# Kernel tuning notes

Measured on AMD Instinct MI355X. Metric: run time of the kernel, lower is better.

## Reference

```python
import jax, jax.numpy as jnp
import numpy as np

# Static graph structure: gene nodes first, GO-term nodes last (mask is sorted).
N_GENE, N_GOID = 40000, 10000
N = N_GENE + N_GOID
E = 800000
INPUT_DIM, H1, H2, OUT_DIM, GOID_DIM = 1280, 256, 128, 64, 4096


def setup_inputs() -> dict:
    key = jax.random.key(0)
    ks = jax.random.split(key, 16)
    s = 0.02
    return {
        "x": jax.random.normal(ks[0], (N, GOID_DIM), jnp.float32),
        "edge_index": jax.random.randint(ks[1], (2, E), 0, N),
        "mask": jnp.concatenate([jnp.ones(N_GENE, bool), jnp.zeros(N_GOID, bool)]),
        # goid_dnn: Linear(4096,1024) -> ReLU -> Linear(1024,INPUT_DIM) -> ReLU
        "Wd1": jax.random.normal(ks[2], (GOID_DIM, 1024), jnp.float32) * s,
        "bd1": jnp.zeros((1024,), jnp.float32),
        "Wd2": jax.random.normal(ks[3], (1024, INPUT_DIM), jnp.float32) * s,
        "bd2": jnp.zeros((INPUT_DIM,), jnp.float32),
        # GCNConv layers
        "W1": jax.random.normal(ks[4], (INPUT_DIM, H1), jnp.float32) * s,
        "b1": jnp.zeros((H1,), jnp.float32),
        "W2": jax.random.normal(ks[5], (H1, H2), jnp.float32) * s,
        "b2": jnp.zeros((H2,), jnp.float32),
        # goid projections
        "Wp1": jax.random.normal(ks[6], (INPUT_DIM, H1), jnp.float32) * s,
        "bp1": jnp.zeros((H1,), jnp.float32),
        "Wp2": jax.random.normal(ks[7], (H1, H2), jnp.float32) * s,
        "bp2": jnp.zeros((H2,), jnp.float32),
        # final fc
        "Wf": jax.random.normal(ks[8], (H2, OUT_DIM), jnp.float32) * s,
        "bf": jnp.zeros((OUT_DIM,), jnp.float32),
    }


def gcn_conv(x, W, b, src, dst):
    """PyG GCNConv: xW, then sym-normalized (A + I) aggregation, then bias."""
    # degree over targets with self-loops already appended to (src, dst)
    deg = jax.ops.segment_sum(jnp.ones_like(dst, x.dtype), dst, num_segments=N)
    dinv = jnp.where(deg > 0, jax.lax.rsqrt(deg), 0.0)
    norm = dinv[src] * dinv[dst]                       # [E+N]
    xw = x @ W                                          # [N, F_out]
    msg = xw[src] * norm[:, None]                       # gather-scale, [E+N, F_out]
    return jax.ops.segment_sum(msg, dst, num_segments=N) + b


def reference(x, edge_index, mask, Wd1, bd1, Wd2, bd2, W1, b1, W2, b2,
              Wp1, bp1, Wp2, bp2, Wf, bf):
    del mask  # structurally: first N_GENE rows are genes, rest are GO terms
    loop = jnp.arange(N, dtype=edge_index.dtype)
    src = jnp.concatenate([edge_index[0], loop])
    dst = jnp.concatenate([edge_index[1], loop])

    gene_x = x[:N_GENE, :INPUT_DIM]
    goid_x = x[N_GENE:]
    # goid_dnn runs under torch.no_grad() -> stop_gradient
    goid_t = jax.lax.stop_gradient(
        jax.nn.relu(jax.nn.relu(goid_x @ Wd1 + bd1) @ Wd2 + bd2))

    x_t = jnp.concatenate([gene_x, goid_t], axis=0)      # [N, INPUT_DIM]
    h1 = jax.nn.relu(gcn_conv(x_t, W1, b1, src, dst))    # dropout disabled (eval)
    p1 = goid_t @ Wp1 + bp1                              # goid_proj1
    h1 = h1.at[N_GENE:].set(p1)                          # masked scatter assign
    h2 = jax.nn.relu(gcn_conv(h1, W2, b2, src, dst))
    h2 = h2.at[N_GENE:].set(p1 @ Wp2 + bp2)              # goid_proj2(goid_proj1(...))
    return h2 @ Wf + bf                                  # [N, OUT_DIM]
```

## Files before the change

### kernel.cpp

```cpp
#include <hip/hip_runtime.h>

constexpr int kNGene = 40000;
constexpr int kNGoid = 10000;
constexpr int kN     = 50000;
constexpr int kE     = 800000;
constexpr int kInDim = 1280;
constexpr int kH1    = 256;
constexpr int kH2    = 128;
constexpr int kOut   = 64;
constexpr int kGDim  = 4096;
constexpr int kD1    = 1024;

typedef short bf16x8 __attribute__((ext_vector_type(8)));
typedef float f32x4  __attribute__((ext_vector_type(4)));

static __device__ __forceinline__ short f2bf(float f) {
  union { float f; unsigned u; } v; v.f = f;
  unsigned r = v.u + 0x7FFF + ((v.u >> 16) & 1);
  return (short)(r >> 16);
}
static __device__ __forceinline__ float bf2f(short s) {
  union { unsigned u; float f; } v;
  v.u = ((unsigned)(unsigned short)s) << 16;
  return v.f;
}
static __device__ __forceinline__ void gld16(const void* g, void* l) {
  __builtin_amdgcn_global_load_lds(
      (const __attribute__((address_space(1))) void*)g,
      (__attribute__((address_space(3))) void*)l, 16, 0, 0);
}
template <int N>
static __device__ __forceinline__ void wait_barrier() {
  if constexpr (N == 0)      asm volatile("s_waitcnt vmcnt(0)" ::: "memory");
  else if constexpr (N == 3) asm volatile("s_waitcnt vmcnt(3)" ::: "memory");
  else                       asm volatile("s_waitcnt vmcnt(4)" ::: "memory");
  __builtin_amdgcn_s_barrier();
  asm volatile("" ::: "memory");
}

constexpr int kCvtBlocks   = 20000;
constexpr int kTransBlocks = 6088;
constexpr int kInitBlocks  = 196;

__global__ __launch_bounds__(256)
void k_prep(const float* __restrict__ goid_x, short* __restrict__ goidx_bf,
            const float* __restrict__ Wd1, short* __restrict__ Wd1t,
            const float* __restrict__ Wd2, short* __restrict__ Wd2t,
            const float* __restrict__ W1,  short* __restrict__ W1t,
            const float* __restrict__ Wp1, short* __restrict__ Wp1t,
            const float* __restrict__ W2,  short* __restrict__ W2t,
            const float* __restrict__ Wp2, short* __restrict__ Wp2t,
            const float* __restrict__ Wf,  short* __restrict__ Wft,
            float* __restrict__ deg, int* __restrict__ gcount)
{
  __shared__ float t[32][33];
  int b = blockIdx.x;
  if (b < kCvtBlocks) {
    int idx = b * 256 + threadIdx.x;
    int r = idx >> 9;
    int c = (idx & 511) << 3;
    const float* sp = goid_x + (size_t)r * kGDim + c;
    float4 v0 = *reinterpret_cast<const float4*>(sp);
    float4 v1 = *reinterpret_cast<const float4*>(sp + 4);
    bf16x8 o;
    o[0]=f2bf(v0.x); o[1]=f2bf(v0.y); o[2]=f2bf(v0.z); o[3]=f2bf(v0.w);
    o[4]=f2bf(v1.x); o[5]=f2bf(v1.y); o[6]=f2bf(v1.z); o[7]=f2bf(v1.w);
    *reinterpret_cast<bf16x8*>(goidx_bf + (size_t)r * kGDim + c) = o;
    return;
  }
  if (b >= kCvtBlocks + kTransBlocks) {
    int i = (b - kCvtBlocks - kTransBlocks) * 256 + threadIdx.x;
    if (i < kN) deg[i] = 1.0f;
    if (i == 0) *gcount = 0;
    return;
  }
  int b2 = b - kCvtBlocks;
  const float* W; short* Wt; int K, N, bi;
  if (b2 < 4096)      { W = Wd1; Wt = Wd1t; K = 4096; N = 1024; bi = b2; }
  else if (b2 < 5376) { W = Wd2; Wt = Wd2t; K = 1024; N = 1280; bi = b2 - 4096; }
  else if (b2 < 5696) { W = W1;  Wt = W1t;  K = 1280; N = 256;  bi = b2 - 5376; }
  else if (b2 < 6016) { W = Wp1; Wt = Wp1t; K = 1280; N = 256;  bi = b2 - 5696; }
  else if (b2 < 6048) { W = W2;  Wt = W2t;  K = 256;  N = 128;  bi = b2 - 6016; }
  else if (b2 < 6080) { W = Wp2; Wt = Wp2t; K = 256;  N = 128;  bi = b2 - 6048; }
  else                { W = Wf;  Wt = Wft;  K = 128;  N = 64;   bi = b2 - 6080; }
  int nbx = N >> 5;
  int n0 = (bi % nbx) * 32, k0 = (bi / nbx) * 32;
  int tx = threadIdx.x & 31, ty = threadIdx.x >> 5;
#pragma unroll
  for (int p = 0; p < 4; ++p)
    t[ty + 8 * p][tx] = W[(size_t)(k0 + ty + 8 * p) * N + n0 + tx];
  __syncthreads();
#pragma unroll
  for (int p = 0; p < 4; ++p)
    Wt[(size_t)(n0 + ty + 8 * p) * K + k0 + tx] = f2bf(t[tx][ty + 8 * p]);
}

__global__ void k_deg_hist(const int* __restrict__ ei, float* __restrict__ deg) {
  int e = blockIdx.x * blockDim.x + threadIdx.x;
  if (e < kE) atomicAdd(&deg[ei[kE + e]], 1.0f);
}
__global__ void k_rowassign(const float* __restrict__ deg, int* __restrict__ rowstart,
                            int* __restrict__ cursor, int* __restrict__ gcount) {
  int i = blockIdx.x * blockDim.x + threadIdx.x;
  int lane = threadIdx.x & 63;
  int c = (i < kNGene) ? ((int)deg[i] - 1) : 0;
  int incl = c;
#pragma unroll
  for (int off = 1; off < 64; off <<= 1) {
    int t = __shfl_up(incl, off, 64);
    if (lane >= off) incl += t;
  }
  int total = __shfl(incl, 63, 64);
  int base = 0;
  if (lane == 63) base = atomicAdd(gcount, total);
  base = __shfl(base, 63, 64);
  if (i < kNGene) {
    int s = base + incl - c;
    rowstart[i] = s;
    cursor[i] = s;
  }
}
__global__ void k_fill(const int* __restrict__ ei, const float* __restrict__ deg,
                       int* __restrict__ cursor, int2* __restrict__ edges) {
  int e = blockIdx.x * blockDim.x + threadIdx.x;
  if (e >= kE) return;
  int dst = ei[kE + e];
  if (dst >= kNGene) return;
  int src = ei[e];
  int pos = atomicAdd(&cursor[dst], 1);
  float nrm = rsqrtf(deg[src] * deg[dst]);
  edges[pos] = make_int2(src, __float_as_int(nrm));
}

template <int F, int OBF>
__global__ __launch_bounds__(256)
void k_gather_bf(const short* __restrict__ xw, const float* __restrict__ deg,
                 const int* __restrict__ rowstart, const int2* __restrict__ edges,
                 const float* __restrict__ bias, void* __restrict__ hv) {
  constexpr int VEC = F / 64;
  int row = (blockIdx.x * blockDim.x + threadIdx.x) >> 6;
  int lane = threadIdx.x & 63;
  if (row >= kNGene) return;
  float dg = deg[row];
  float inv = 1.0f / dg;
  float acc[VEC];
  {
    const short* xr = xw + (size_t)row * F + lane * VEC;
    if constexpr (VEC == 4) {
      short4 s = *reinterpret_cast<const short4*>(xr);
      acc[0] = bf2f(s.x) * inv; acc[1] = bf2f(s.y) * inv;
      acc[2] = bf2f(s.z) * inv; acc[3] = bf2f(s.w) * inv;
    } else {
      short2 s = *reinterpret_cast<const short2*>(xr);
      acc[0] = bf2f(s.x) * inv; acc[1] = bf2f(s.y) * inv;
    }
  }
  const int2* ep = edges + rowstart[row];
  int n = (int)dg - 1;
  int e = 0;
  for (; e + 1 < n; e += 2) {
    int2 p0 = ep[e], p1 = ep[e + 1];
    float n0 = __int_as_float(p0.y), n1 = __int_as_float(p1.y);
    const short* x0 = xw + (size_t)p0.x * F + lane * VEC;
    const short* x1 = xw + (size_t)p1.x * F + lane * VEC;
    if constexpr (VEC == 4) {
      short4 s0 = *reinterpret_cast<const short4*>(x0);
      short4 s1 = *reinterpret_cast<const short4*>(x1);
      acc[0] += bf2f(s0.x) * n0; acc[1] += bf2f(s0.y) * n0;
      acc[2] += bf2f(s0.z) * n0; acc[3] += bf2f(s0.w) * n0;
      acc[0] += bf2f(s1.x) * n1; acc[1] += bf2f(s1.y) * n1;
      acc[2] += bf2f(s1.z) * n1; acc[3] += bf2f(s1.w) * n1;
    } else {
      short2 s0 = *reinterpret_cast<const short2*>(x0);
      short2 s1 = *reinterpret_cast<const short2*>(x1);
      acc[0] += bf2f(s0.x) * n0; acc[1] += bf2f(s0.y) * n0;
      acc[0] += bf2f(s1.x) * n1; acc[1] += bf2f(s1.y) * n1;
    }
  }
  if (e < n) {
    int2 p0 = ep[e];
    float n0 = __int_as_float(p0.y);
    const short* x0 = xw + (size_t)p0.x * F + lane * VEC;
    if constexpr (VEC == 4) {
      short4 s0 = *reinterpret_cast<const short4*>(x0);
      acc[0] += bf2f(s0.x) * n0; acc[1] += bf2f(s0.y) * n0;
      acc[2] += bf2f(s0.z) * n0; acc[3] += bf2f(s0.w) * n0;
    } else {
      short2 s0 = *reinterpret_cast<const short2*>(x0);
      acc[0] += bf2f(s0.x) * n0; acc[1] += bf2f(s0.y) * n0;
    }
  }
#pragma unroll
  for (int v = 0; v < VEC; ++v) acc[v] = fmaxf(acc[v] + bias[lane * VEC + v], 0.f);
  if constexpr (OBF) {
    short* hp = (short*)hv + (size_t)row * F + lane * VEC;
    if constexpr (VEC == 4) {
      short4 o; o.x = f2bf(acc[0]); o.y = f2bf(acc[1]); o.z = f2bf(acc[2]); o.w = f2bf(acc[3]);
      *reinterpret_cast<short4*>(hp) = o;
    } else {
      short2 o; o.x = f2bf(acc[0]); o.y = f2bf(acc[1]);
      *reinterpret_cast<short2*>(hp) = o;
    }
  } else {
    float* hp = (float*)hv + (size_t)row * F + lane * VEC;
    if constexpr (VEC == 4) {
      float4 o; o.x = acc[0]; o.y = acc[1]; o.z = acc[2]; o.w = acc[3];
      *reinterpret_cast<float4*>(hp) = o;
    } else {
      float2 o; o.x = acc[0]; o.y = acc[1];
      *reinterpret_cast<float2*>(hp) = o;
    }
  }
}

template <int RELU, int OBF>
__global__ __launch_bounds__(256)
void k_gemm_bf16a(const short* __restrict__ A, int lda,
                  const short* __restrict__ Bt,
                  const float* __restrict__ bias,
                  void* __restrict__ Cv, int ldc,
                  int M, int K)
{
  __shared__ __align__(16) short As[3][128 * 32];
  __shared__ __align__(16) short Bs[3][128 * 32];
  const int tid  = threadIdx.x;
  const int lane = tid & 63;
  const int wid  = tid >> 6;
  const int wr = wid >> 1, wc = wid & 1;
  const int row0 = blockIdx.y * 128;
  const int col0 = blockIdx.x * 128;
  const int l15 = lane & 15, l4 = lane >> 4;
  const int srow = lane >> 2;
  const int schunk = (lane & 3) ^ ((lane >> 3) & 3);
  const int rslot8 = (l4 ^ ((l15 >> 1) & 3)) * 8;

  f32x4 acc[4][4] = {};

  auto stage = [&](int buf, int k0) {
#pragma unroll
    for (int q = 0; q < 2; ++q) {
      int seg = wid * 2 + q;
      int r = seg * 16 + srow;
      int grow = row0 + r;
      if (grow >= M) grow = M - 1;
      gld16(A + (size_t)grow * lda + k0 + schunk * 8, &As[buf][seg * 512]);
      int gcol = col0 + r;
      gld16(Bt + (size_t)gcol * K + k0 + schunk * 8, &Bs[buf][seg * 512]);
    }
  };

  const int nt = K >> 5;
  stage(0, 0);
  if (nt > 1) { stage(1, 32); wait_barrier<4>(); }
  else        { wait_barrier<0>(); }

  for (int t = 0; t < nt; ++t) {
    if (t + 2 < nt) stage((t + 2) % 3, (t + 2) * 32);
    const int cur = t % 3;
    bf16x8 af[4], bfr[4];
#pragma unroll
    for (int m = 0; m < 4; ++m)
      af[m] = *reinterpret_cast<bf16x8*>(&As[cur][(wr * 64 + m * 16 + l15) * 32 + rslot8]);
#pragma unroll
    for (int n = 0; n < 4; ++n)
      bfr[n] = *reinterpret_cast<bf16x8*>(&Bs[cur][(wc * 64 + n * 16 + l15) * 32 + rslot8]);
#pragma unroll
    for (int m = 0; m < 4; ++m)
#pragma unroll
      for (int n = 0; n < 4; ++n)
        acc[m][n] = __builtin_amdgcn_mfma_f32_16x16x32_bf16(af[m], bfr[n], acc[m][n], 0, 0, 0);
    if (t + 1 < nt) {
      if (t + 2 < nt) wait_barrier<4>(); else wait_barrier<0>();
    }
  }

#pragma unroll
  for (int n = 0; n < 4; ++n) {
    int col = col0 + wc * 64 + n * 16 + l15;
    float bv = bias ? bias[col] : 0.f;
#pragma unroll
    for (int m = 0; m < 4; ++m) {
      int rb = row0 + wr * 64 + m * 16 + l4 * 4;
#pragma unroll
      for (int e = 0; e < 4; ++e) {
        int r = rb + e;
        if (r < M) {
          float v = acc[m][n][e] + bv;
          if (RELU) v = fmaxf(v, 0.f);
          size_t idx = (size_t)r * ldc + col;
          if constexpr (OBF) ((short*)Cv)[idx] = f2bf(v);
          else               ((float*)Cv)[idx] = v;
        }
      }
    }
  }
}

template <int RELU, int OBF>
__global__ __launch_bounds__(512)
void k_gemm_wide(const short* __restrict__ A, int lda,
                 const short* __restrict__ Bt,
                 const float* __restrict__ bias,
                 void* __restrict__ Cv, int ldc,
                 int M, int K)
{
  __shared__ __align__(16) short As[3][128 * 32];
  __shared__ __align__(16) short Bs[3][256 * 32];
  const int tid  = threadIdx.x;
  const int lane = tid & 63;
  const int wid  = tid >> 6;
  const int wr = wid >> 2, wc = wid & 3;
  int nwg = gridDim.x * gridDim.y;
  int b0 = blockIdx.y * gridDim.x + blockIdx.x;
  int qq = nwg >> 3, rr = nwg & 7, xcd = b0 & 7, j = b0 >> 3;
  int swz = ((xcd < rr) ? xcd * (qq + 1) : rr * (qq + 1) + (xcd - rr) * qq) + j;
  const int row0 = (swz / gridDim.x) * 128;
  const int col0 = (swz % gridDim.x) * 256;
  const int l15 = lane & 15, l4 = lane >> 4;
  const int srow = lane >> 2;
  const int schunk = (lane & 3) ^ ((lane >> 3) & 3);
  const int rslot8 = (l4 ^ ((l15 >> 1) & 3)) * 8;

  f32x4 acc[4][4] = {};

  auto stage = [&](int buf, int k0) {
#pragma unroll
    for (int q = 0; q < 3; ++q) {
      int s = wid * 3 + q;
      if (s < 8) {
        int grow = row0 + s * 16 + srow;
        if (grow >= M) grow = M - 1;
        gld16(A + (size_t)grow * lda + k0 + schunk * 8, &As[buf][s * 512]);
      } else {
        int gcol = col0 + (s - 8) * 16 + srow;
        gld16(Bt + (size_t)gcol * K + k0 + schunk * 8, &Bs[buf][(s - 8) * 512]);
      }
    }
  };

  const int nt = K >> 5;
  stage(0, 0);
  if (nt > 1) { stage(1, 32); wait_barrier<3>(); }
  else        { wait_barrier<0>(); }

  for (int t = 0; t < nt; ++t) {
    if (t + 2 < nt) stage((t + 2) % 3, (t + 2) * 32);
    const int cur = t % 3;
    bf16x8 af[4], bfr[4];
#pragma unroll
    for (int m = 0; m < 4; ++m)
      af[m] = *reinterpret_cast<bf16x8*>(&As[cur][(wr * 64 + m * 16 + l15) * 32 + rslot8]);
#pragma unroll
    for (int n = 0; n < 4; ++n)
      bfr[n] = *reinterpret_cast<bf16x8*>(&Bs[cur][(wc * 64 + n * 16 + l15) * 32 + rslot8]);
#pragma unroll
    for (int m = 0; m < 4; ++m)
#pragma unroll
      for (int n = 0; n < 4; ++n)
        acc[m][n] = __builtin_amdgcn_mfma_f32_16x16x32_bf16(af[m], bfr[n], acc[m][n], 0, 0, 0);
    if (t + 1 < nt) {
      if (t + 2 < nt) wait_barrier<3>(); else wait_barrier<0>();
    }
  }

#pragma unroll
  for (int n = 0; n < 4; ++n) {
    int col = col0 + wc * 64 + n * 16 + l15;
    float bv = bias ? bias[col] : 0.f;
#pragma unroll
    for (int m = 0; m < 4; ++m) {
      int rb = row0 + wr * 64 + m * 16 + l4 * 4;
#pragma unroll
      for (int e = 0; e < 4; ++e) {
        int r = rb + e;
        if (r < M) {
          float v = acc[m][n][e] + bv;
          if (RELU) v = fmaxf(v, 0.f);
          size_t idx = (size_t)r * ldc + col;
          if constexpr (OBF) ((short*)Cv)[idx] = f2bf(v);
          else               ((float*)Cv)[idx] = v;
        }
      }
    }
  }
}

__global__ __launch_bounds__(512)
void k_combo_wide(const short* __restrict__ A, int lda,
                  const short* __restrict__ Bt,
                  const float* __restrict__ bp1,
                  short* __restrict__ X1, short* __restrict__ H1,
                  int M, int K)
{
  __shared__ __align__(16) short As[2][128 * 32];
  __shared__ __align__(16) short Bs[2][256 * 32];
  const int tid  = threadIdx.x;
  const int lane = tid & 63;
  const int wid  = tid >> 6;
  const int wr = wid >> 2, wc = wid & 3;
  const int row0 = blockIdx.y * 128;
  const int col0 = blockIdx.x * 256;
  const int l15 = lane & 15, l4 = lane >> 4;
  const int srow = lane >> 2;
  const int schunk = (lane & 3) ^ ((lane >> 3) & 3);
  const int rslot8 = (l4 ^ ((l15 >> 1) & 3)) * 8;

  f32x4 acc[4][4] = {};

  auto stage = [&](int buf, int k0) {
#pragma unroll
    for (int q = 0; q < 3; ++q) {
      int s = wid * 3 + q;
      if (s < 8) {
        int grow = row0 + s * 16 + srow;
        if (grow >= M) grow = M - 1;
        gld16(A + (size_t)grow * lda + k0 + schunk * 8, &As[buf][s * 512]);
      } else {
        int gcol = col0 + (s - 8) * 16 + srow;
        gld16(Bt + (size_t)gcol * K + k0 + schunk * 8, &Bs[buf][(s - 8) * 512]);
      }
    }
  };

  stage(0, 0);
  __syncthreads();
  int cur = 0;
  for (int k0 = 0; k0 < K; k0 += 32) {
    if (k0 + 32 < K) stage(cur ^ 1, k0 + 32);
    bf16x8 af[4], bfr[4];
#pragma unroll
    for (int m = 0; m < 4; ++m)
      af[m] = *reinterpret_cast<bf16x8*>(&As[cur][(wr * 64 + m * 16 + l15) * 32 + rslot8]);
#pragma unroll
    for (int n = 0; n < 4; ++n)
      bfr[n] = *reinterpret_cast<bf16x8*>(&Bs[cur][(wc * 64 + n * 16 + l15) * 32 + rslot8]);
#pragma unroll
    for (int m = 0; m < 4; ++m)
#pragma unroll
      for (int n = 0; n < 4; ++n)
        acc[m][n] = __builtin_amdgcn_mfma_f32_16x16x32_bf16(af[m], bfr[n], acc[m][n], 0, 0, 0);
    __syncthreads();
    cur ^= 1;
  }

  const int is_p1 = (col0 >= 256);
  short* dstp = is_p1 ? H1 : X1;
#pragma unroll
  for (int n = 0; n < 4; ++n) {
    int cl = wc * 64 + n * 16 + l15;
    float bv = is_p1 ? bp1[cl] : 0.f;
#pragma unroll
    for (int m = 0; m < 4; ++m) {
      int rb = row0 + wr * 64 + m * 16 + l4 * 4;
#pragma unroll
      for (int e = 0; e < 4; ++e) {
        int r = rb + e;
        if (r < M) dstp[(size_t)r * 256 + cl] = f2bf(acc[m][n][e] + bv);
      }
    }
  }
}

__global__ __launch_bounds__(512)
void k_gemm_gene(const float* __restrict__ A, int lda,
                 const short* __restrict__ Bt,
                 short* __restrict__ C,
                 int M, int K)
{
  __shared__ short As[2][128 * 40];
  __shared__ __align__(16) short Bs[2][256 * 32];
  const int tid  = threadIdx.x;
  const int lane = tid & 63;
  const int wid  = tid >> 6;
  const int wr = wid >> 2, wc = wid & 3;
  const int row0 = blockIdx.x * 128;
  const int l15 = lane & 15, l4 = lane >> 4;
  const int sr = tid >> 2, sc = tid & 3;
  const int srow = lane >> 2;
  const int schunk = (lane & 3) ^ ((lane >> 3) & 3);
  const int rslot8 = (l4 ^ ((l15 >> 1) & 3)) * 8;

  f32x4 acc[4][4] = {};

  auto stageB = [&](int buf, int k0) {
#pragma unroll
    for (int q = 0; q < 2; ++q) {
      int seg = wid * 2 + q;
      int gcol = seg * 16 + srow;
      gld16(Bt + (size_t)gcol * K + k0 + schunk * 8, &Bs[buf][seg * 512]);
    }
  };
  auto stageA = [&](int buf, int k0) {
    int grow = row0 + sr;
    float4 v0 = make_float4(0.f,0.f,0.f,0.f), v1 = v0;
    if (grow < M) {
      const float* ap = A + (size_t)grow * lda + k0 + sc * 8;
      v0 = *reinterpret_cast<const float4*>(ap);
      v1 = *reinterpret_cast<const float4*>(ap + 4);
    }
    bf16x8 t;
    t[0]=f2bf(v0.x); t[1]=f2bf(v0.y); t[2]=f2bf(v0.z); t[3]=f2bf(v0.w);
    t[4]=f2bf(v1.x); t[5]=f2bf(v1.y); t[6]=f2bf(v1.z); t[7]=f2bf(v1.w);
    *reinterpret_cast<bf16x8*>(&As[buf][sr * 40 + sc * 8]) = t;
  };

  stageB(0, 0); stageA(0, 0);
  __syncthreads();
  int cur = 0;
  for (int k0 = 0; k0 < K; k0 += 32) {
    if (k0 + 32 < K) { stageB(cur ^ 1, k0 + 32); stageA(cur ^ 1, k0 + 32); }
    bf16x8 af[4], bfr[4];
#pragma unroll
    for (int m = 0; m < 4; ++m)
      af[m] = *reinterpret_cast<bf16x8*>(&As[cur][(wr * 64 + m * 16 + l15) * 40 + l4 * 8]);
#pragma unroll
    for (int n = 0; n < 4; ++n)
      bfr[n] = *reinterpret_cast<bf16x8*>(&Bs[cur][(wc * 64 + n * 16 + l15) * 32 + rslot8]);
#pragma unroll
    for (int m = 0; m < 4; ++m)
#pragma unroll
      for (int n = 0; n < 4; ++n)
        acc[m][n] = __builtin_amdgcn_mfma_f32_16x16x32_bf16(af[m], bfr[n], acc[m][n], 0, 0, 0);
    __syncthreads();
    cur ^= 1;
  }

#pragma unroll
  for (int n = 0; n < 4; ++n) {
    int col = wc * 64 + n * 16 + l15;
#pragma unroll
    for (int m = 0; m < 4; ++m) {
      int rb = row0 + wr * 64 + m * 16 + l4 * 4;
#pragma unroll
      for (int e = 0; e < 4; ++e) {
        int r = rb + e;
        if (r < M) C[(size_t)r * 256 + col] = f2bf(acc[m][n][e]);
      }
    }
  }
}

__global__ __launch_bounds__(256)
void k_gemm_out(const short* __restrict__ A,
                const short* __restrict__ Bt,
                const float* __restrict__ bias,
                float* __restrict__ C,
                int M)
{
  __shared__ __align__(16) short As[2][256 * 32];
  __shared__ __align__(16) short Bs[2][64 * 32];
  const int tid  = threadIdx.x;
  const int lane = tid & 63;
  const int wid  = tid >> 6;
  const int row0 = blockIdx.x * 256;
  const int l15 = lane & 15, l4 = lane >> 4;
  const int srow = lane >> 2;
  const int schunk = (lane & 3) ^ ((lane >> 3) & 3);
  const int rslot8 = (l4 ^ ((l15 >> 1) & 3)) * 8;

  f32x4 acc[4][4] = {};

  auto stage = [&](int buf, int k0) {
#pragma unroll
    for (int q = 0; q < 4; ++q) {
      int seg = wid * 4 + q;
      int grow = row0 + seg * 16 + srow;
      if (grow >= M) grow = M - 1;
      gld16(A + (size_t)grow * 128 + k0 + schunk * 8, &As[buf][seg * 512]);
    }
    int gcol = wid * 16 + srow;
    gld16(Bt + (size_t)gcol * 128 + k0 + schunk * 8, &Bs[buf][wid * 512]);
  };

  stage(0, 0);
  __syncthreads();
  int cur = 0;
  for (int k0 = 0; k0 < 128; k0 += 32) {
    if (k0 + 32 < 128) stage(cur ^ 1, k0 + 32);
    bf16x8 af[4], bfr[4];
#pragma unroll
    for (int m = 0; m < 4; ++m)
      af[m] = *reinterpret_cast<bf16x8*>(&As[cur][(wid * 64 + m * 16 + l15) * 32 + rslot8]);
#pragma unroll
    for (int n = 0; n < 4; ++n)
      bfr[n] = *reinterpret_cast<bf16x8*>(&Bs[cur][(n * 16 + l15) * 32 + rslot8]);
#pragma unroll
    for (int m = 0; m < 4; ++m)
#pragma unroll
      for (int n = 0; n < 4; ++n)
        acc[m][n] = __builtin_amdgcn_mfma_f32_16x16x32_bf16(af[m], bfr[n], acc[m][n], 0, 0, 0);
    __syncthreads();
    cur ^= 1;
  }

#pragma unroll
  for (int n = 0; n < 4; ++n) {
    int col = n * 16 + l15;
    float bv = bias[col];
#pragma unroll
    for (int m = 0; m < 4; ++m) {
      int rb = row0 + wid * 64 + m * 16 + l4 * 4;
#pragma unroll
      for (int e = 0; e < 4; ++e) {
        int r = rb + e;
        if (r < M) C[(size_t)r * 64 + col] = acc[m][n][e] + bv;
      }
    }
  }
}

extern "C" void kernel_launch(void* const* d_in, const int* in_sizes, int n_in,
                              void* d_out, int out_size, void* d_ws, size_t ws_size,
                              hipStream_t stream) {
  const float* x   = (const float*)d_in[0];
  const int*   ei  = (const int*)d_in[1];
  const float* Wd1 = (const float*)d_in[3];
  const float* bd1 = (const float*)d_in[4];
  const float* Wd2 = (const float*)d_in[5];
  const float* bd2 = (const float*)d_in[6];
  const float* W1  = (const float*)d_in[7];
  const float* b1  = (const float*)d_in[8];
  const float* W2  = (const float*)d_in[9];
  const float* b2  = (const float*)d_in[10];
  const float* Wp1 = (const float*)d_in[11];
  const float* bp1 = (const float*)d_in[12];
  const float* Wp2 = (const float*)d_in[13];
  const float* bp2 = (const float*)d_in[14];
  const float* Wf  = (const float*)d_in[15];
  const float* bf_ = (const float*)d_in[16];
  float* out = (float*)d_out;
  float* ws  = (float*)d_ws;

  short* goidx_bf = (short*)(ws + 0);
  short* goidt_bf = (short*)(ws + 20480000);
  short* h1tmp_bf = (short*)(ws + 26880000);
  short* Wd1t = (short*)(ws + 32000000);
  short* Wd2t = (short*)(ws + 34097152);
  short* W1t  = (short*)(ws + 34752512);
  short* Wp1t = (short*)(ws + 34916352);
  short* W2t  = (short*)(ws + 35080192);
  short* xw1_bf = (short*)(ws + 35100000);
  short* h1bf   = (short*)(ws + 41500000);
  short* xw2_bf = (short*)(ws + 50460000);
  short* h2bf   = (short*)(ws + 53660000);
  float* deg    = ws + 60060000;
  int*   rowstart = (int*)(ws + 60150016);
  int*   cursor   = (int*)(ws + 60190016);
  int2*  edges    = (int2*)(ws + 60230016);
  int*   gcount   = (int*)(ws + 61830016);
  short* Wp2t = (short*)(ws + 61830032);
  short* Wft  = (short*)(ws + 61846416);

  const float* gene_x = x;
  const float* goid_x = x + (size_t)kNGene * kGDim;

  auto gb = [](int M, int Ncol) { return dim3((unsigned)(Ncol / 128), (unsigned)((M + 127) / 128)); };
  auto gw = [](int M, int Ncol) { return dim3((unsigned)(Ncol / 256), (unsigned)((M + 127) / 128)); };

  k_prep<<<kCvtBlocks + kTransBlocks + kInitBlocks, 256, 0, stream>>>(
      goid_x, goidx_bf, Wd1, Wd1t, Wd2, Wd2t, W1, W1t, Wp1, Wp1t,
      W2, W2t, Wp2, Wp2t, Wf, Wft, deg, gcount);

  k_deg_hist<<<(kE + 255) / 256, 256, 0, stream>>>(ei, deg);
  k_rowassign<<<(kNGene + 255) / 256, 256, 0, stream>>>(deg, rowstart, cursor, gcount);
  k_fill<<<(kE + 255) / 256, 256, 0, stream>>>(ei, deg, cursor, edges);

  k_gemm_wide<1,1><<<gw(kNGoid, kD1), 512, 0, stream>>>(goidx_bf, kGDim, Wd1t, bd1,
                                                        h1tmp_bf, kD1, kNGoid, kGDim);
  k_gemm_wide<1,1><<<gw(kNGoid, kInDim), 512, 0, stream>>>(h1tmp_bf, kD1, Wd2t, bd2,
                                                           goidt_bf, kInDim, kNGoid, kD1);

  k_gemm_gene<<<dim3((kNGene + 127) / 128), 512, 0, stream>>>(gene_x, kGDim, W1t,
                                                              xw1_bf, kNGene, kInDim);

  k_combo_wide<<<dim3(2, (kNGoid + 127) / 128), 512, 0, stream>>>(
      goidt_bf, kInDim, W1t , bp1,
      xw1_bf + (size_t)kNGene * kH1, h1bf + (size_t)kNGene * kH1,
      kNGoid, kInDim);

  k_gather_bf<kH1,1><<<(kNGene * 64 + 255) / 256, 256, 0, stream>>>(
      xw1_bf, deg, rowstart, edges, b1, h1bf);

  k_gemm_bf16a<0,1><<<gb(kN, kH2), 256, 0, stream>>>(h1bf, kH1, W2t, nullptr,
                                                     xw2_bf, kH2, kN, kH1);

  k_gather_bf<kH2,1><<<(kNGene * 64 + 255) / 256, 256, 0, stream>>>(
      xw2_bf, deg, rowstart, edges, b2, h2bf);
  k_gemm_bf16a<0,1><<<gb(kNGoid, kH2), 256, 0, stream>>>(
      h1bf + (size_t)kNGene * kH1, kH1, Wp2t, bp2,
      h2bf + (size_t)kNGene * kH2, kH2, kNGoid, kH1);

  k_gemm_out<<<(kN + 255) / 256, 256, 0, stream>>>(h2bf, Wft, bf_, out, kN);
}
```

Before: 603.3 us.

## Merge independent GEMMs and graph-build kernels into combined heterogeneous launches

Independent stages are packed into single launches with per-block dispatch: the Wd1 GEMM, gene GEMM and degree histogram share one kernel; the Wd2 GEMM shares one with row assignment; the combo GEMM shares one with CSR fill; and the W2 and Wp2 GEMMs are merged. This cuts launch count and lets the light atomic work overlap the GEMMs instead of running serially. In exchange, the Wd GEMMs lose their triple-buffered pipeline and use a double-buffered loop with full barriers. Dynamic shared memory sized for the largest branch may also lower occupancy for the light blocks.

```diff
diff --git a/kernel.cpp b/kernel.cpp
--- a/kernel.cpp
+++ b/kernel.cpp
@@ -95,13 +95,16 @@
     Wt[(size_t)(n0 + ty + 8 * p) * K + k0 + tx] = f2bf(t[tx][ty + 8 * p]);
 }
 
-__global__ void k_deg_hist(const int* __restrict__ ei, float* __restrict__ deg) {
-  int e = blockIdx.x * blockDim.x + threadIdx.x;
+static __device__ void dev_hist(const int* __restrict__ ei, float* __restrict__ deg,
+                                int bid) {
+  int e = bid * 512 + threadIdx.x;
   if (e < kE) atomicAdd(&deg[ei[kE + e]], 1.0f);
 }
-__global__ void k_rowassign(const float* __restrict__ deg, int* __restrict__ rowstart,
-                            int* __restrict__ cursor, int* __restrict__ gcount) {
-  int i = blockIdx.x * blockDim.x + threadIdx.x;
+static __device__ void dev_rowassign(const float* __restrict__ deg,
+                                     int* __restrict__ rowstart,
+                                     int* __restrict__ cursor,
+                                     int* __restrict__ gcount, int bid) {
+  int i = bid * 512 + threadIdx.x;
   int lane = threadIdx.x & 63;
   int c = (i < kNGene) ? ((int)deg[i] - 1) : 0;
   int incl = c;
@@ -120,9 +123,10 @@
     cursor[i] = s;
   }
 }
-__global__ void k_fill(const int* __restrict__ ei, const float* __restrict__ deg,
-                       int* __restrict__ cursor, int2* __restrict__ edges) {
-  int e = blockIdx.x * blockDim.x + threadIdx.x;
+static __device__ void dev_fill(const int* __restrict__ ei, const float* __restrict__ deg,
+                                int* __restrict__ cursor, int2* __restrict__ edges,
+                                int bid) {
+  int e = bid * 512 + threadIdx.x;
   if (e >= kE) return;
   int dst = ei[kE + e];
   if (dst >= kNGene) return;
@@ -214,21 +218,21 @@
 }
 
 template <int RELU, int OBF>
-__global__ __launch_bounds__(256)
-void k_gemm_bf16a(const short* __restrict__ A, int lda,
-                  const short* __restrict__ Bt,
-                  const float* __restrict__ bias,
-                  void* __restrict__ Cv, int ldc,
-                  int M, int K)
-{
-  __shared__ __align__(16) short As[3][128 * 32];
-  __shared__ __align__(16) short Bs[3][128 * 32];
+static __device__ void dev_wide(const short* __restrict__ A, int lda,
+                                const short* __restrict__ Bt,
+                                const float* __restrict__ bias,
+                                void* __restrict__ Cv, int ldc,
+                                int M, int K, int b0, int nbx, int nwg,
+                                short* As, short* Bs)
+{
   const int tid  = threadIdx.x;
   const int lane = tid & 63;
   const int wid  = tid >> 6;
-  const int wr = wid >> 1, wc = wid & 1;
-  const int row0 = blockIdx.y * 128;
-  const int col0 = blockIdx.x * 128;
+  const int wr = wid >> 2, wc = wid & 3;
+  int qq = nwg >> 3, rr = nwg & 7, xcd = b0 & 7, j = b0 >> 3;
+  int swz = ((xcd < rr) ? xcd * (qq + 1) : rr * (qq + 1) + (xcd - rr) * qq) + j;
+  const int row0 = (swz / nbx) * 128;
+  const int col0 = (swz % nbx) * 256;
   const int l15 = lane & 15, l4 = lane >> 4;
   const int srow = lane >> 2;
   const int schunk = (lane & 3) ^ ((lane >> 3) & 3);
@@ -238,40 +242,38 @@
 
   auto stage = [&](int buf, int k0) {
 #pragma unroll
-    for (int q = 0; q < 2; ++q) {
-      int seg = wid * 2 + q;
-      int r = seg * 16 + srow;
-      int grow = row0 + r;
-      if (grow >= M) grow = M - 1;
-      gld16(A + (size_t)grow * lda + k0 + schunk * 8, &As[buf][seg * 512]);
-      int gcol = col0 + r;
-      gld16(Bt + (size_t)gcol * K + k0 + schunk * 8, &Bs[buf][seg * 512]);
+    for (int q = 0; q < 3; ++q) {
+      int s = wid * 3 + q;
+      if (s < 8) {
+        int grow = row0 + s * 16 + srow;
+        if (grow >= M) grow = M - 1;
+        gld16(A + (size_t)grow * lda + k0 + schunk * 8, As + buf * 4096 + s * 512);
+      } else {
+        int gcol = col0 + (s - 8) * 16 + srow;
+        gld16(Bt + (size_t)gcol * K + k0 + schunk * 8, Bs + buf * 8192 + (s - 8) * 512);
+      }
     }
   };
 
-  const int nt = K >> 5;
   stage(0, 0);
-  if (nt > 1) { stage(1, 32); wait_barrier<4>(); }
-  else        { wait_barrier<0>(); }
-
-  for (int t = 0; t < nt; ++t) {
-    if (t + 2 < nt) stage((t + 2) % 3, (t + 2) * 32);
-    const int cur = t % 3;
+  __syncthreads();
+  int cur = 0;
+  for (int k0 = 0; k0 < K; k0 += 32) {
+    if (k0 + 32 < K) stage(cur ^ 1, k0 + 32);
     bf16x8 af[4], bfr[4];
 #pragma unroll
     for (int m = 0; m < 4; ++m)
-      af[m] = *reinterpret_cast<bf16x8*>(&As[cur][(wr * 64 + m * 16 + l15) * 32 + rslot8]);
+      af[m] = *reinterpret_cast<bf16x8*>(As + cur * 4096 + (wr * 64 + m * 16 + l15) * 32 + rslot8);
 #pragma unroll
     for (int n = 0; n < 4; ++n)
-      bfr[n] = *reinterpret_cast<bf16x8*>(&Bs[cur][(wc * 64 + n * 16 + l15) * 32 + rslot8]);
+      bfr[n] = *reinterpret_cast<bf16x8*>(Bs + cur * 8192 + (wc * 64 + n * 16 + l15) * 32 + rslot8);
 #pragma unroll
     for (int m = 0; m < 4; ++m)
 #pragma unroll
       for (int n = 0; n < 4; ++n)
         acc[m][n] = __builtin_amdgcn_mfma_f32_16x16x32_bf16(af[m], bfr[n], acc[m][n], 0, 0, 0);
-    if (t + 1 < nt) {
-      if (t + 2 < nt) wait_barrier<4>(); else wait_barrier<0>();
-    }
+    __syncthreads();
+    cur ^= 1;
   }
 
 #pragma unroll
@@ -296,26 +298,95 @@
   }
 }
 
-template <int RELU, int OBF>
-__global__ __launch_bounds__(512)
-void k_gemm_wide(const short* __restrict__ A, int lda,
-                 const short* __restrict__ Bt,
-                 const float* __restrict__ bias,
-                 void* __restrict__ Cv, int ldc,
-                 int M, int K)
-{
-  __shared__ __align__(16) short As[3][128 * 32];
-  __shared__ __align__(16) short Bs[3][256 * 32];
+static __device__ void dev_gene(const float* __restrict__ A, int lda,
+                                const short* __restrict__ Bt,
+                                short* __restrict__ C, int M, int K,
+                                int bx, short* As, short* Bs)
+{
   const int tid  = threadIdx.x;
   const int lane = tid & 63;
   const int wid  = tid >> 6;
   const int wr = wid >> 2, wc = wid & 3;
-  int nwg = gridDim.x * gridDim.y;
-  int b0 = blockIdx.y * gridDim.x + blockIdx.x;
-  int qq = nwg >> 3, rr = nwg & 7, xcd = b0 & 7, j = b0 >> 3;
-  int swz = ((xcd < rr) ? xcd * (qq + 1) : rr * (qq + 1) + (xcd - rr) * qq) + j;
-  const int row0 = (swz / gridDim.x) * 128;
-  const int col0 = (swz % gridDim.x) * 256;
+  const int row0 = bx * 128;
+  const int l15 = lane & 15, l4 = lane >> 4;
+  const int sr = tid >> 2, sc = tid & 3;
+  const int srow = lane >> 2;
+  const int schunk = (lane & 3) ^ ((lane >> 3) & 3);
+  const int rslot8 = (l4 ^ ((l15 >> 1) & 3)) * 8;
+
+  f32x4 acc[4][4] = {};
+
+  auto stageB = [&](int buf, int k0) {
+#pragma unroll
+    for (int q = 0; q < 2; ++q) {
+      int seg = wid * 2 + q;
+      int gcol = seg * 16 + srow;
+      gld16(Bt + (size_t)gcol * K + k0 + schunk * 8, Bs + buf * 8192 + seg * 512);
+    }
+  };
+  auto stageA = [&](int buf, int k0) {
+    int grow = row0 + sr;
+    float4 v0 = make_float4(0.f,0.f,0.f,0.f), v1 = v0;
+    if (grow < M) {
+      const float* ap = A + (size_t)grow * lda + k0 + sc * 8;
+      v0 = *reinterpret_cast<const float4*>(ap);
+      v1 = *reinterpret_cast<const float4*>(ap + 4);
+    }
+    bf16x8 t;
+    t[0]=f2bf(v0.x); t[1]=f2bf(v0.y); t[2]=f2bf(v0.z); t[3]=f2bf(v0.w);
+    t[4]=f2bf(v1.x); t[5]=f2bf(v1.y); t[6]=f2bf(v1.z); t[7]=f2bf(v1.w);
+    *reinterpret_cast<bf16x8*>(As + buf * 5120 + sr * 40 + sc * 8) = t;
+  };
+
+  stageB(0, 0); stageA(0, 0);
+  __syncthreads();
+  int cur = 0;
+  for (int k0 = 0; k0 < K; k0 += 32) {
+    if (k0 + 32 < K) { stageB(cur ^ 1, k0 + 32); stageA(cur ^ 1, k0 + 32); }
+    bf16x8 af[4], bfr[4];
+#pragma unroll
+    for (int m = 0; m < 4; ++m)
+      af[m] = *reinterpret_cast<bf16x8*>(As + cur * 5120 + (wr * 64 + m * 16 + l15) * 40 + l4 * 8);
+#pragma unroll
+    for (int n = 0; n < 4; ++n)
+      bfr[n] = *reinterpret_cast<bf16x8*>(Bs + cur * 8192 + (wc * 64 + n * 16 + l15) * 32 + rslot8);
+#pragma unroll
+    for (int m = 0; m < 4; ++m)
+#pragma unroll
+      for (int n = 0; n < 4; ++n)
+        acc[m][n] = __builtin_amdgcn_mfma_f32_16x16x32_bf16(af[m], bfr[n], acc[m][n], 0, 0, 0);
+    __syncthreads();
+    cur ^= 1;
+  }
+
+#pragma unroll
+  for (int n = 0; n < 4; ++n) {
+    int col = wc * 64 + n * 16 + l15;
+#pragma unroll
+    for (int m = 0; m < 4; ++m) {
+      int rb = row0 + wr * 64 + m * 16 + l4 * 4;
+#pragma unroll
+      for (int e = 0; e < 4; ++e) {
+        int r = rb + e;
+        if (r < M) C[(size_t)r * 256 + col] = f2bf(acc[m][n][e]);
+      }
+    }
+  }
+}
+
+static __device__ void dev_combo(const short* __restrict__ A, int lda,
+                                 const short* __restrict__ Bt,
+                                 const float* __restrict__ bp1,
+                                 short* __restrict__ X1, short* __restrict__ H1,
+                                 int M, int K, int bx, int by,
+                                 short* As, short* Bs)
+{
+  const int tid  = threadIdx.x;
+  const int lane = tid & 63;
+  const int wid  = tid >> 6;
+  const int wr = wid >> 2, wc = wid & 3;
+  const int row0 = by * 128;
+  const int col0 = bx * 256;
   const int l15 = lane & 15, l4 = lane >> 4;
   const int srow = lane >> 2;
   const int schunk = (lane & 3) ^ ((lane >> 3) & 3);
@@ -330,17 +401,90 @@
       if (s < 8) {
         int grow = row0 + s * 16 + srow;
         if (grow >= M) grow = M - 1;
-        gld16(A + (size_t)grow * lda + k0 + schunk * 8, &As[buf][s * 512]);
+        gld16(A + (size_t)grow * lda + k0 + schunk * 8, As + buf * 4096 + s * 512);
       } else {
         int gcol = col0 + (s - 8) * 16 + srow;
-        gld16(Bt + (size_t)gcol * K + k0 + schunk * 8, &Bs[buf][(s - 8) * 512]);
+        gld16(Bt + (size_t)gcol * K + k0 + schunk * 8, Bs + buf * 8192 + (s - 8) * 512);
       }
+    }
+  };
+
+  stage(0, 0);
+  __syncthreads();
+  int cur = 0;
+  for (int k0 = 0; k0 < K; k0 += 32) {
+    if (k0 + 32 < K) stage(cur ^ 1, k0 + 32);
+    bf16x8 af[4], bfr[4];
+#pragma unroll
+    for (int m = 0; m < 4; ++m)
+      af[m] = *reinterpret_cast<bf16x8*>(As + cur * 4096 + (wr * 64 + m * 16 + l15) * 32 + rslot8);
+#pragma unroll
+    for (int n = 0; n < 4; ++n)
+      bfr[n] = *reinterpret_cast<bf16x8*>(Bs + cur * 8192 + (wc * 64 + n * 16 + l15) * 32 + rslot8);
+#pragma unroll
+    for (int m = 0; m < 4; ++m)
+#pragma unroll
+      for (int n = 0; n < 4; ++n)
+        acc[m][n] = __builtin_amdgcn_mfma_f32_16x16x32_bf16(af[m], bfr[n], acc[m][n], 0, 0, 0);
+    __syncthreads();
+    cur ^= 1;
+  }
+
+  const int is_p1 = (col0 >= 256);
+  short* dstp = is_p1 ? H1 : X1;
+#pragma unroll
+  for (int n = 0; n < 4; ++n) {
+    int cl = wc * 64 + n * 16 + l15;
+    float bv = is_p1 ? bp1[cl] : 0.f;
+#pragma unroll
+    for (int m = 0; m < 4; ++m) {
+      int rb = row0 + wr * 64 + m * 16 + l4 * 4;
+#pragma unroll
+      for (int e = 0; e < 4; ++e) {
+        int r = rb + e;
+        if (r < M) dstp[(size_t)r * 256 + cl] = f2bf(acc[m][n][e] + bv);
+      }
+    }
+  }
+}
+
+template <int RELU, int OBF>
+static __device__ void dev_bf16a(const short* __restrict__ A, int lda,
+                                 const short* __restrict__ Bt,
+                                 const float* __restrict__ bias,
+                                 void* __restrict__ Cv, int ldc,
+                                 int M, int K, int bx, int by,
+                                 short* As, short* Bs)
+{
+  const int tid  = threadIdx.x;
+  const int lane = tid & 63;
+  const int wid  = tid >> 6;
+  const int wr = wid >> 1, wc = wid & 1;
+  const int row0 = by * 128;
+  const int col0 = bx * 128;
+  const int l15 = lane & 15, l4 = lane >> 4;
+  const int srow = lane >> 2;
+  const int schunk = (lane & 3) ^ ((lane >> 3) & 3);
+  const int rslot8 = (l4 ^ ((l15 >> 1) & 3)) * 8;
+
+  f32x4 acc[4][4] = {};
+
+  auto stage = [&](int buf, int k0) {
+#pragma unroll
+    for (int q = 0; q < 2; ++q) {
+      int seg = wid * 2 + q;
+      int r = seg * 16 + srow;
+      int grow = row0 + r;
+      if (grow >= M) grow = M - 1;
+      gld16(A + (size_t)grow * lda + k0 + schunk * 8, As + buf * 4096 + seg * 512);
+      int gcol = col0 + r;
+      gld16(Bt + (size_t)gcol * K + k0 + schunk * 8, Bs + buf * 4096 + seg * 512);
     }
   };
 
   const int nt = K >> 5;
   stage(0, 0);
-  if (nt > 1) { stage(1, 32); wait_barrier<3>(); }
+  if (nt > 1) { stage(1, 32); wait_barrier<4>(); }
   else        { wait_barrier<0>(); }
 
   for (int t = 0; t < nt; ++t) {
@@ -349,17 +493,17 @@
     bf16x8 af[4], bfr[4];
 #pragma unroll
     for (int m = 0; m < 4; ++m)
-      af[m] = *reinterpret_cast<bf16x8*>(&As[cur][(wr * 64 + m * 16 + l15) * 32 + rslot8]);
+      af[m] = *reinterpret_cast<bf16x8*>(As + cur * 4096 + (wr * 64 + m * 16 + l15) * 32 + rslot8);
 #pragma unroll
     for (int n = 0; n < 4; ++n)
-      bfr[n] = *reinterpret_cast<bf16x8*>(&Bs[cur][(wc * 64 + n * 16 + l15) * 32 + rslot8]);
+      bfr[n] = *reinterpret_cast<bf16x8*>(Bs + cur * 4096 + (wc * 64 + n * 16 + l15) * 32 + rslot8);
 #pragma unroll
     for (int m = 0; m < 4; ++m)
 #pragma unroll
       for (int n = 0; n < 4; ++n)
         acc[m][n] = __builtin_amdgcn_mfma_f32_16x16x32_bf16(af[m], bfr[n], acc[m][n], 0, 0, 0);
     if (t + 1 < nt) {
-      if (t + 2 < nt) wait_barrier<3>(); else wait_barrier<0>();
+      if (t + 2 < nt) wait_barrier<4>(); else wait_barrier<0>();
     }
   }
 
@@ -385,158 +529,74 @@
   }
 }
 
+constexpr int kWd1Blocks  = 316;
+constexpr int kGeneBlocks = 313;
+constexpr int kHistBlocks = 1563;
+constexpr int kWd2Blocks  = 395;
+constexpr int kRowBlocks  = 79;
+constexpr int kComboBlocks = 158;
+constexpr int kXw2Blocks  = 391;
+constexpr int kWp2Blocks  = 79;
+
 __global__ __launch_bounds__(512)
-void k_combo_wide(const short* __restrict__ A, int lda,
-                  const short* __restrict__ Bt,
-                  const float* __restrict__ bp1,
-                  short* __restrict__ X1, short* __restrict__ H1,
-                  int M, int K)
-{
-  __shared__ __align__(16) short As[2][128 * 32];
-  __shared__ __align__(16) short Bs[2][256 * 32];
-  const int tid  = threadIdx.x;
-  const int lane = tid & 63;
-  const int wid  = tid >> 6;
-  const int wr = wid >> 2, wc = wid & 3;
-  const int row0 = blockIdx.y * 128;
-  const int col0 = blockIdx.x * 256;
-  const int l15 = lane & 15, l4 = lane >> 4;
-  const int srow = lane >> 2;
-  const int schunk = (lane & 3) ^ ((lane >> 3) & 3);
-  const int rslot8 = (l4 ^ ((l15 >> 1) & 3)) * 8;
-
-  f32x4 acc[4][4] = {};
-
-  auto stage = [&](int buf, int k0) {
-#pragma unroll
-    for (int q = 0; q < 3; ++q) {
-      int s = wid * 3 + q;
-      if (s < 8) {
-        int grow = row0 + s * 16 + srow;
-        if (grow >= M) grow = M - 1;
-        gld16(A + (size_t)grow * lda + k0 + schunk * 8, &As[buf][s * 512]);
-      } else {
-        int gcol = col0 + (s - 8) * 16 + srow;
-        gld16(Bt + (size_t)gcol * K + k0 + schunk * 8, &Bs[buf][(s - 8) * 512]);
-      }
-    }
-  };
-
-  stage(0, 0);
-  __syncthreads();
-  int cur = 0;
-  for (int k0 = 0; k0 < K; k0 += 32) {
-    if (k0 + 32 < K) stage(cur ^ 1, k0 + 32);
-    bf16x8 af[4], bfr[4];
-#pragma unroll
-    for (int m = 0; m < 4; ++m)
-      af[m] = *reinterpret_cast<bf16x8*>(&As[cur][(wr * 64 + m * 16 + l15) * 32 + rslot8]);
-#pragma unroll
-    for (int n = 0; n < 4; ++n)
-      bfr[n] = *reinterpret_cast<bf16x8*>(&Bs[cur][(wc * 64 + n * 16 + l15) * 32 + rslot8]);
-#pragma unroll
-    for (int m = 0; m < 4; ++m)
-#pragma unroll
-      for (int n = 0; n < 4; ++n)
-        acc[m][n] = __builtin_amdgcn_mfma_f32_16x16x32_bf16(af[m], bfr[n], acc[m][n], 0, 0, 0);
-    __syncthreads();
-    cur ^= 1;
-  }
-
-  const int is_p1 = (col0 >= 256);
-  short* dstp = is_p1 ? H1 : X1;
-#pragma unroll
-  for (int n = 0; n < 4; ++n) {
-    int cl = wc * 64 + n * 16 + l15;
-    float bv = is_p1 ? bp1[cl] : 0.f;
-#pragma unroll
-    for (int m = 0; m < 4; ++m) {
-      int rb = row0 + wr * 64 + m * 16 + l4 * 4;
-#pragma unroll
-      for (int e = 0; e < 4; ++e) {
-        int r = rb + e;
-        if (r < M) dstp[(size_t)r * 256 + cl] = f2bf(acc[m][n][e] + bv);
-      }
-    }
+void k_big1(const short* goidx_bf, const short* Wd1t, const float* bd1, short* h1tmp_bf,
+            const float* gene_x, const short* W1t, short* xw1_bf,
+            const int* ei, float* deg)
+{
+  extern __shared__ short smem[];
+  int b = blockIdx.x;
+  if (b < kWd1Blocks) {
+    dev_wide<1,1>(goidx_bf, kGDim, Wd1t, bd1, h1tmp_bf, kD1, kNGoid, kGDim,
+                  b, 4, kWd1Blocks, smem, smem + 2 * 4096);
+  } else if (b < kWd1Blocks + kGeneBlocks) {
+    dev_gene(gene_x, kGDim, W1t, xw1_bf, kNGene, kInDim,
+             b - kWd1Blocks, smem, smem + 2 * 5120);
+  } else {
+    dev_hist(ei, deg, b - kWd1Blocks - kGeneBlocks);
   }
 }
 
 __global__ __launch_bounds__(512)
-void k_gemm_gene(const float* __restrict__ A, int lda,
-                 const short* __restrict__ Bt,
-                 short* __restrict__ C,
-                 int M, int K)
-{
-  __shared__ short As[2][128 * 40];
-  __shared__ __align__(16) short Bs[2][256 * 32];
-  const int tid  = threadIdx.x;
-  const int lane = tid & 63;
-  const int wid  = tid >> 6;
-  const int wr = wid >> 2, wc = wid & 3;
-  const int row0 = blockIdx.x * 128;
-  const int l15 = lane & 15, l4 = lane >> 4;
-  const int sr = tid >> 2, sc = tid & 3;
-  const int srow = lane >> 2;
-  const int schunk = (lane & 3) ^ ((lane >> 3) & 3);
-  const int rslot8 = (l4 ^ ((l15 >> 1) & 3)) * 8;
-
-  f32x4 acc[4][4] = {};
-
-  auto stageB = [&](int buf, int k0) {
-#pragma unroll
-    for (int q = 0; q < 2; ++q) {
-      int seg = wid * 2 + q;
-      int gcol = seg * 16 + srow;
-      gld16(Bt + (size_t)gcol * K + k0 + schunk * 8, &Bs[buf][seg * 512]);
-    }
-  };
-  auto stageA = [&](int buf, int k0) {
-    int grow = row0 + sr;
-    float4 v0 = make_float4(0.f,0.f,0.f,0.f), v1 = v0;
-    if (grow < M) {
-      const float* ap = A + (size_t)grow * lda + k0 + sc * 8;
-      v0 = *reinterpret_cast<const float4*>(ap);
-      v1 = *reinterpret_cast<const float4*>(ap + 4);
-    }
-    bf16x8 t;
-    t[0]=f2bf(v0.x); t[1]=f2bf(v0.y); t[2]=f2bf(v0.z); t[3]=f2bf(v0.w);
-    t[4]=f2bf(v1.x); t[5]=f2bf(v1.y); t[6]=f2bf(v1.z); t[7]=f2bf(v1.w);
-    *reinterpret_cast<bf16x8*>(&As[buf][sr * 40 + sc * 8]) = t;
-  };
-
-  stageB(0, 0); stageA(0, 0);
-  __syncthreads();
-  int cur = 0;
-  for (int k0 = 0; k0 < K; k0 += 32) {
-    if (k0 + 32 < K) { stageB(cur ^ 1, k0 + 32); stageA(cur ^ 1, k0 + 32); }
-    bf16x8 af[4], bfr[4];
-#pragma unroll
-    for (int m = 0; m < 4; ++m)
-      af[m] = *reinterpret_cast<bf16x8*>(&As[cur][(wr * 64 + m * 16 + l15) * 40 + l4 * 8]);
-#pragma unroll
-    for (int n = 0; n < 4; ++n)
-      bfr[n] = *reinterpret_cast<bf16x8*>(&Bs[cur][(wc * 64 + n * 16 + l15) * 32 + rslot8]);
-#pragma unroll
-    for (int m = 0; m < 4; ++m)
-#pragma unroll
-      for (int n = 0; n < 4; ++n)
-        acc[m][n] = __builtin_amdgcn_mfma_f32_16x16x32_bf16(af[m], bfr[n], acc[m][n], 0, 0, 0);
-    __syncthreads();
-    cur ^= 1;
-  }
-
-#pragma unroll
-  for (int n = 0; n < 4; ++n) {
-    int col = wc * 64 + n * 16 + l15;
-#pragma unroll
-    for (int m = 0; m < 4; ++m) {
-      int rb = row0 + wr * 64 + m * 16 + l4 * 4;
-#pragma unroll
-      for (int e = 0; e < 4; ++e) {
-        int r = rb + e;
-        if (r < M) C[(size_t)r * 256 + col] = f2bf(acc[m][n][e]);
-      }
-    }
+void k_big2(const short* h1tmp_bf, const short* Wd2t, const float* bd2, short* goidt_bf,
+            const float* deg, int* rowstart, int* cursor, int* gcount)
+{
+  extern __shared__ short smem[];
+  int b = blockIdx.x;
+  if (b < kWd2Blocks) {
+    dev_wide<1,1>(h1tmp_bf, kD1, Wd2t, bd2, goidt_bf, kInDim, kNGoid, kD1,
+                  b, 5, kWd2Blocks, smem, smem + 2 * 4096);
+  } else {
+    dev_rowassign(deg, rowstart, cursor, gcount, b - kWd2Blocks);
+  }
+}
+
+__global__ __launch_bounds__(512)
+void k_big3(const short* goidt_bf, const short* Wcomb, const float* bp1,
+            short* X1, short* H1,
+            const int* ei, const float* deg, int* cursor, int2* edges)
+{
+  extern __shared__ short smem[];
+  int b = blockIdx.x;
+  if (b < kComboBlocks) {
+    dev_combo(goidt_bf, kInDim, Wcomb, bp1, X1, H1, kNGoid, kInDim,
+              b & 1, b >> 1, smem, smem + 2 * 4096);
+  } else {
+    dev_fill(ei, deg, cursor, edges, b - kComboBlocks);
+  }
+}
+
+__global__ __launch_bounds__(256)
+void k_xwp(const short* h1bf, const short* W2t, short* xw2_bf,
+           const short* h1goid, const short* Wp2t, const float* bp2, short* h2goid)
+{
+  extern __shared__ short smem[];
+  int b = blockIdx.x;
+  if (b < kXw2Blocks) {
+    dev_bf16a<0,1>(h1bf, kH1, W2t, nullptr, xw2_bf, kH2, kN, kH1,
+                   0, b, smem, smem + 3 * 4096);
+  } else {
+    dev_bf16a<0,1>(h1goid, kH1, Wp2t, bp2, h2goid, kH2, kNGoid, kH1,
+                   0, b - kXw2Blocks, smem, smem + 3 * 4096);
   }
 }
 
@@ -654,41 +714,30 @@
   const float* gene_x = x;
   const float* goid_x = x + (size_t)kNGene * kGDim;
 
-  auto gb = [](int M, int Ncol) { return dim3((unsigned)(Ncol / 128), (unsigned)((M + 127) / 128)); };
-  auto gw = [](int M, int Ncol) { return dim3((unsigned)(Ncol / 256), (unsigned)((M + 127) / 128)); };
-
   k_prep<<<kCvtBlocks + kTransBlocks + kInitBlocks, 256, 0, stream>>>(
       goid_x, goidx_bf, Wd1, Wd1t, Wd2, Wd2t, W1, W1t, Wp1, Wp1t,
       W2, W2t, Wp2, Wp2t, Wf, Wft, deg, gcount);
 
-  k_deg_hist<<<(kE + 255) / 256, 256, 0, stream>>>(ei, deg);
-  k_rowassign<<<(kNGene + 255) / 256, 256, 0, stream>>>(deg, rowstart, cursor, gcount);
-  k_fill<<<(kE + 255) / 256, 256, 0, stream>>>(ei, deg, cursor, edges);
-
-  k_gemm_wide<1,1><<<gw(kNGoid, kD1), 512, 0, stream>>>(goidx_bf, kGDim, Wd1t, bd1,
-                                                        h1tmp_bf, kD1, kNGoid, kGDim);
-  k_gemm_wide<1,1><<<gw(kNGoid, kInDim), 512, 0, stream>>>(h1tmp_bf, kD1, Wd2t, bd2,
-                                                           goidt_bf, kInDim, kNGoid, kD1);
-
-  k_gemm_gene<<<dim3((kNGene + 127) / 128), 512, 0, stream>>>(gene_x, kGDim, W1t,
-                                                              xw1_bf, kNGene, kInDim);
-
-  k_combo_wide<<<dim3(2, (kNGoid + 127) / 128), 512, 0, stream>>>(
-      goidt_bf, kInDim, W1t , bp1,
+  k_big1<<<kWd1Blocks + kGeneBlocks + kHistBlocks, 512, 53248, stream>>>(
+      goidx_bf, Wd1t, bd1, h1tmp_bf, gene_x, W1t, xw1_bf, ei, deg);
+
+  k_big2<<<kWd2Blocks + kRowBlocks, 512, 49152, stream>>>(
+      h1tmp_bf, Wd2t, bd2, goidt_bf, deg, rowstart, cursor, gcount);
+
+  k_big3<<<kComboBlocks + kHistBlocks, 512, 49152, stream>>>(
+      goidt_bf, W1t , bp1,
       xw1_bf + (size_t)kNGene * kH1, h1bf + (size_t)kNGene * kH1,
-      kNGoid, kInDim);
+      ei, deg, cursor, edges);
 
   k_gather_bf<kH1,1><<<(kNGene * 64 + 255) / 256, 256, 0, stream>>>(
       xw1_bf, deg, rowstart, edges, b1, h1bf);
 
-  k_gemm_bf16a<0,1><<<gb(kN, kH2), 256, 0, stream>>>(h1bf, kH1, W2t, nullptr,
-                                                     xw2_bf, kH2, kN, kH1);
+  k_xwp<<<kXw2Blocks + kWp2Blocks, 256, 49152, stream>>>(
+      h1bf, W2t, xw2_bf,
+      h1bf + (size_t)kNGene * kH1, Wp2t, bp2, h2bf + (size_t)kNGene * kH2);
 
   k_gather_bf<kH2,1><<<(kNGene * 64 + 255) / 256, 256, 0, stream>>>(
       xw2_bf, deg, rowstart, edges, b2, h2bf);
-  k_gemm_bf16a<0,1><<<gb(kNGoid, kH2), 256, 0, stream>>>(
-      h1bf + (size_t)kNGene * kH1, kH1, Wp2t, bp2,
-      h2bf + (size_t)kNGene * kH2, kH2, kNGoid, kH1);
 
   k_gemm_out<<<(kN + 255) / 256, 256, 0, stream>>>(h2bf, Wft, bf_, out, kN);
 }
```

Measured after the change: 573.0 us. 1.05x faster.
